# Performance work log

Measured on AMD Instinct MI355X. Metric: run time of the kernel, lower is better.

Reference implementation:

```python
import jax, jax.numpy as jnp
import numpy as np

N, E, IN, HID, H, G, OUT = 50000, 800000, 128, 96, 8, 64, 10
D = HID // H  # per-head dim = 12


def setup_inputs() -> dict:
    key = jax.random.key(0)
    ks = jax.random.split(key, 24)
    s = 0.1
    inp = {
        'x': jax.random.normal(ks[0], (N, IN), jnp.float32),
        'src': jax.random.randint(ks[1], (E,), 0, N, jnp.int32),
        'dst': jax.random.randint(ks[2], (E,), 0, N, jnp.int32),
        'graph_id': jax.random.randint(ks[3], (N,), 0, G, jnp.int32),
        # GraphConv layers (norm='both', weight + bias)
        'W1': jax.random.normal(ks[4], (IN, HID), jnp.float32) * s,
        'b1': jnp.zeros((HID,), jnp.float32),
        'W2': jax.random.normal(ks[5], (HID, HID), jnp.float32) * s,
        'b2': jnp.zeros((HID,), jnp.float32),
        # 3 GATv2 layers, stacked params
        'Ws': jax.random.normal(ks[6], (3, HID, HID), jnp.float32) * s,
        'bs': jnp.zeros((3, HID), jnp.float32),
        'Wd': jax.random.normal(ks[7], (3, HID, HID), jnp.float32) * s,
        'bd': jnp.zeros((3, HID), jnp.float32),
        'attn': jax.random.normal(ks[8], (3, H, D), jnp.float32) * s,
        # classifier MLP (dropout is identity at inference)
        'Wc1': jax.random.normal(ks[9], (HID, HID), jnp.float32) * s,
        'bc1': jnp.zeros((HID,), jnp.float32),
        'Wc2': jax.random.normal(ks[10], (HID, HID // 2), jnp.float32) * s,
        'bc2': jnp.zeros((HID // 2,), jnp.float32),
        'Wc3': jax.random.normal(ks[11], (HID // 2, OUT), jnp.float32) * s,
        'bc3': jnp.zeros((OUT,), jnp.float32),
    }
    return inp


def _graph_conv(h, W, b, src, dst):
    # DGL GraphConv, norm='both', allow_zero_in_degree (degrees clamped to >=1)
    ones = jnp.ones((E,), h.dtype)
    deg_out = jnp.clip(jax.ops.segment_sum(ones, src, N), 1.0)
    deg_in = jnp.clip(jax.ops.segment_sum(ones, dst, N), 1.0)
    h = (h * (deg_out ** -0.5)[:, None]) @ W          # [N, out]
    agg = jax.ops.segment_sum(h[src], dst, N)          # sum over in-edges
    return agg * (deg_in ** -0.5)[:, None] + b


def _gatv2(h, Ws, bs, Wd, bd, attn, src, dst):
    fs = (h @ Ws + bs).reshape(N, H, D)
    fd = (h @ Wd + bd).reshape(N, H, D)
    e = jax.nn.leaky_relu(fs[src] + fd[dst], 0.2)      # [E, H, D]
    logits = jnp.einsum('ehd,hd->eh', e, attn)         # [E, H]
    # edge softmax over incoming edges of each dst node
    m = jax.ops.segment_max(logits, dst, N)            # [N, H]
    ex = jnp.exp(logits - m[dst])
    den = jax.ops.segment_sum(ex, dst, N)              # [N, H]
    a = ex / den[dst]                                  # [E, H]
    rst = jax.ops.segment_sum(a[:, :, None] * fs[src], dst, N)  # [N, H, D]
    return jax.nn.relu(rst).reshape(N, HID)            # activation=relu, then view


def reference(x, src, dst, graph_id, W1, b1, W2, b2, Ws, bs, Wd, bd, attn,
              Wc1, bc1, Wc2, bc2, Wc3, bc3):
    h = jax.nn.relu(_graph_conv(x, W1, b1, src, dst))
    h = jax.nn.relu(_graph_conv(h, W2, b2, src, dst))
    for i in range(3):
        h = _gatv2(h, Ws[i], bs[i], Wd[i], bd[i], attn[i], src, dst)
    # dgl.max_nodes: per-graph max readout
    hg = jax.ops.segment_max(h, graph_id, G)           # [G, HID]
    z = jax.nn.relu(hg @ Wc1 + bc1)
    z = jax.nn.relu(z @ Wc2 + bc2)
    return z @ Wc3 + bc3                               # [G, OUT]
```

## Files before the change

### kernel.cpp

```cpp
#include <hip/hip_runtime.h>
#include <hip/hip_bf16.h>

#define Nn 50000
#define Ee 800000
#define INF_ 128
#define HIDF 96
#define HH 8
#define DD 12
#define GG 64
#define OUTF 10

#define SCAN_CHUNK 512
#define SCAN_BLOCKS ((Nn + SCAN_CHUNK - 1) / SCAN_CHUNK)
#define NSB ((Nn + 255) / 256)
#define RB 128

#define HCHK 256
#define HCHKE (Ee / HCHK)
#define NW 12512
#define DBIN 64

__global__ __launch_bounds__(512) void hist_lds(const int* __restrict__ src,
                                                const int* __restrict__ dst,
                                                unsigned int* __restrict__ partS,
                                                unsigned int* __restrict__ partD,
                                                unsigned char* __restrict__ edge_slot) {
    __shared__ unsigned int hS[NW];
    __shared__ unsigned int hD[NW];
    int b = blockIdx.x, t = threadIdx.x;
    for (int i = t; i < NW; i += 512) { hS[i] = 0u; hD[i] = 0u; }
    __syncthreads();
    int base = b * HCHKE;
    for (int i = t; i < HCHKE; i += 512) {
        int d = dst[base + i];
        unsigned int old = atomicAdd(&hD[d >> 2], 1u << ((d & 3) * 8));
        edge_slot[base + i] = (unsigned char)((old >> ((d & 3) * 8)) & 0xFFu);
        int s = src[base + i];
        atomicAdd(&hS[s >> 2], 1u << ((s & 3) * 8));
    }
    __syncthreads();
    for (int i = t; i < NW; i += 512) {
        partD[(size_t)b * NW + i] = hD[i];
        partS[(size_t)b * NW + i] = hS[i];
    }
}

__global__ __launch_bounds__(256) void hist_scan(unsigned int* __restrict__ partD,
                                                 const unsigned int* __restrict__ partS,
                                                 int* __restrict__ cnt_in,
                                                 float* __restrict__ degI_is,
                                                 float* __restrict__ degO_is,
                                                 int* __restrict__ dcnt) {
    __shared__ int hbin[DBIN];
    int t = threadIdx.x;
    if (t < DBIN) hbin[t] = 0;
    __syncthreads();
    int w = blockIdx.x * 256 + t;
    if (w < NW) {
        unsigned int run = 0u, totS = 0u;
        for (int b = 0; b < HCHK; ++b) {
            size_t idx = (size_t)b * NW + w;
            unsigned int v = partD[idx];
            partD[idx] = run;
            run += v;
            totS += partS[idx];
        }
#pragma unroll
        for (int j = 0; j < 4; ++j) {
            int k = w * 4 + j;
            if (k < Nn) {
                int di = (int)((run >> (j * 8)) & 0xFFu);
                int dо = (int)((totS >> (j * 8)) & 0xFFu);
                cnt_in[k] = di;
                degI_is[k] = rsqrtf((float)max(di, 1));
                degO_is[k] = rsqrtf((float)max(dо, 1));
                atomicAdd(&hbin[DBIN - 1 - min(di, DBIN - 1)], 1);
            }
        }
    }
    __syncthreads();
    if (t < DBIN && hbin[t]) atomicAdd(&dcnt[t], hbin[t]);
}

__global__ __launch_bounds__(256) void scan1_kernel(const int* __restrict__ cnt,
                                                    int* __restrict__ row_start,
                                                    int* __restrict__ blk_sum, int N) {
    __shared__ int part[256];
    int t = threadIdx.x;
    int base = blockIdx.x * SCAN_CHUNK;
    int i0 = base + 2 * t, i1 = i0 + 1;
    int a = (i0 < N) ? cnt[i0] : 0;
    int b = (i1 < N) ? cnt[i1] : 0;
    int s = a + b;
    part[t] = s;
    __syncthreads();
    for (int off = 1; off < 256; off <<= 1) {
        int v = (t >= off) ? part[t - off] : 0;
        __syncthreads();
        part[t] += v;
        __syncthreads();
    }
    int excl = part[t] - s;
    if (i0 < N) row_start[i0] = excl;
    if (i1 < N) row_start[i1] = excl + a;
    if (t == 255) blk_sum[blockIdx.x] = part[255];
}

__global__ __launch_bounds__(128) void scan2_kernel(const int* __restrict__ blk_sum,
                                                    int* __restrict__ blk_off,
                                                    int* __restrict__ row_start,
                                                    const int* __restrict__ dcnt,
                                                    int* __restrict__ dcur, int N) {
    __shared__ int part[128];
    int t = threadIdx.x;
    if (blockIdx.x == 0) {
        int v0 = (t < SCAN_BLOCKS) ? blk_sum[t] : 0;
        part[t] = v0;
        __syncthreads();
        for (int off = 1; off < 128; off <<= 1) {
            int v = (t >= off) ? part[t - off] : 0;
            __syncthreads();
            part[t] += v;
            __syncthreads();
        }
        blk_off[t] = part[t] - v0;
        if (t == 127) row_start[N] = part[127];
    } else {
        int v0 = (t < DBIN) ? dcnt[t] : 0;
        part[t] = v0;
        __syncthreads();
        for (int off = 1; off < DBIN; off <<= 1) {
            int v = (t >= off) ? part[t - off] : 0;
            __syncthreads();
            part[t] += v;
            __syncthreads();
        }
        if (t < DBIN) dcur[t] = part[t] - v0;
    }
}

__global__ __launch_bounds__(256) void scan3_kernel(int* __restrict__ row_start,
                                                    const int* __restrict__ blk_off,
                                                    const int* __restrict__ cnt_in,
                                                    int* __restrict__ dcur,
                                                    int* __restrict__ perm, int N) {
    int t = threadIdx.x;
    if (blockIdx.x < SCAN_BLOCKS) {
        int base = blockIdx.x * SCAN_CHUNK;
        int off = blk_off[blockIdx.x];
        int i0 = base + 2 * t, i1 = i0 + 1;
        if (i0 < N) row_start[i0] += off;
        if (i1 < N) row_start[i1] += off;
    } else {
        __shared__ int lh[DBIN];
        __shared__ int lbase[DBIN];
        if (t < DBIN) lh[t] = 0;
        __syncthreads();
        int n = (blockIdx.x - SCAN_BLOCKS) * 256 + t;
        int bin = 0, lslot = 0;
        if (n < N) {
            bin = DBIN - 1 - min(cnt_in[n], DBIN - 1);
            lslot = atomicAdd(&lh[bin], 1);
        }
        __syncthreads();
        if (t < DBIN) lbase[t] = lh[t] ? atomicAdd(&dcur[t], lh[t]) : 0;
        __syncthreads();
        if (n < N) perm[lbase[bin] + lslot] = n;
    }
}

__global__ __launch_bounds__(512) void fill_kernel(const int* __restrict__ src,
                                                   const int* __restrict__ dst,
                                                   const int* __restrict__ row_start,
                                                   const unsigned int* __restrict__ partD,
                                                   const unsigned char* __restrict__ edge_slot,
                                                   int* __restrict__ csr_src) {
    int b = blockIdx.x, t = threadIdx.x;
    int base = b * HCHKE;
    size_t po = (size_t)b * NW;
    for (int i = t; i < HCHKE; i += 512) {
        int e = base + i;
        int d = dst[e];
        int cb = (int)((partD[po + (d >> 2)] >> ((d & 3) * 8)) & 0xFFu);
        csr_src[row_start[d] + cb + (int)edge_slot[e]] = src[e];
    }
}

__global__ __launch_bounds__(192, 1) void gemm96(const float* __restrict__ A, int K,
                                                 const float* __restrict__ W,
                                                 const float* __restrict__ bias,
                                                 const float* __restrict__ rowScale,
                                                 float* __restrict__ out, int N) {
    __shared__ float W_lds[128 * 96];
    const int t = threadIdx.x;
    const int row0 = blockIdx.x * 64;
    const int tcol = t % 24;
    const int trow = t / 24;

    for (int i = t; i < K * 24; i += 192)
        ((float4*)W_lds)[i] = ((const float4*)W)[i];

    const float* Ap[8];
    float sc[8];
#pragma unroll
    for (int i = 0; i < 8; ++i) {
        int gr = row0 + trow + 8 * i;
        gr = gr < N ? gr : N - 1;
        Ap[i] = A + (size_t)gr * K;
        sc[i] = rowScale ? rowScale[gr] : 1.f;
    }
    float acc[8][4];
#pragma unroll
    for (int i = 0; i < 8; ++i)
#pragma unroll
        for (int j = 0; j < 4; ++j) acc[i][j] = 0.f;

    float4 bufA[8], bufB[8];
#pragma unroll
    for (int i = 0; i < 8; ++i) bufA[i] = *((const float4*)(Ap[i]));

    __syncthreads();

    auto compute = [&](const float4* a, int k) {
#pragma unroll
        for (int kk = 0; kk < 4; ++kk) {
            float4 wv = *((const float4*)(W_lds + (k + kk) * 96 + tcol * 4));
#pragma unroll
            for (int i = 0; i < 8; ++i) {
                float av = ((kk == 0) ? a[i].x : (kk == 1) ? a[i].y
                           : (kk == 2) ? a[i].z : a[i].w) * sc[i];
                acc[i][0] = fmaf(av, wv.x, acc[i][0]);
                acc[i][1] = fmaf(av, wv.y, acc[i][1]);
                acc[i][2] = fmaf(av, wv.z, acc[i][2]);
                acc[i][3] = fmaf(av, wv.w, acc[i][3]);
            }
        }
    };

    for (int k = 0; k + 8 <= K; k += 8) {
#pragma unroll
        for (int i = 0; i < 8; ++i) bufB[i] = *((const float4*)(Ap[i] + k + 4));
        compute(bufA, k);
        if (k + 8 < K) {
#pragma unroll
            for (int i = 0; i < 8; ++i) bufA[i] = *((const float4*)(Ap[i] + k + 8));
        }
        compute(bufB, k + 4);
    }
    float4 b4 = bias ? *((const float4*)(bias + tcol * 4)) : make_float4(0.f, 0.f, 0.f, 0.f);
#pragma unroll
    for (int i = 0; i < 8; ++i) {
        int gr = row0 + trow + 8 * i;
        if (gr < N) {
            float4 o = make_float4(acc[i][0] + b4.x, acc[i][1] + b4.y,
                                   acc[i][2] + b4.z, acc[i][3] + b4.w);
            *((float4*)(out + (size_t)gr * 96 + tcol * 4)) = o;
        }
    }
}

__global__ __launch_bounds__(192, 1) void gemm96x2(const float* __restrict__ A,
                                                   const float* __restrict__ W1_, const float* __restrict__ b1_,
                                                   const float* __restrict__ W2_, const float* __restrict__ b2_,
                                                   float* __restrict__ out1, float* __restrict__ out2, int N) {
    __shared__ float W_lds[2 * 96 * 96];
    const int t = threadIdx.x;
    const int row0 = blockIdx.x * 64;
    const int tcol = t % 24;
    const int trow = t / 24;

    for (int i = t; i < 96 * 24; i += 192) {
        ((float4*)W_lds)[i] = ((const float4*)W1_)[i];
        ((float4*)(W_lds + 96 * 96))[i] = ((const float4*)W2_)[i];
    }

    const float* Ap[8];
#pragma unroll
    for (int i = 0; i < 8; ++i) {
        int gr = row0 + trow + 8 * i;
        gr = gr < N ? gr : N - 1;
        Ap[i] = A + (size_t)gr * 96;
    }
    float acc1[8][4], acc2[8][4];
#pragma unroll
    for (int i = 0; i < 8; ++i)
#pragma unroll
        for (int j = 0; j < 4; ++j) { acc1[i][j] = 0.f; acc2[i][j] = 0.f; }

    float4 bufA[8], bufB[8];
#pragma unroll
    for (int i = 0; i < 8; ++i) bufA[i] = *((const float4*)(Ap[i]));

    __syncthreads();

    auto compute = [&](const float4* a, int k) {
#pragma unroll
        for (int kk = 0; kk < 4; ++kk) {
            float4 wv1 = *((const float4*)(W_lds + (k + kk) * 96 + tcol * 4));
            float4 wv2 = *((const float4*)(W_lds + 96 * 96 + (k + kk) * 96 + tcol * 4));
#pragma unroll
            for (int i = 0; i < 8; ++i) {
                float av = (kk == 0) ? a[i].x : (kk == 1) ? a[i].y : (kk == 2) ? a[i].z : a[i].w;
                acc1[i][0] = fmaf(av, wv1.x, acc1[i][0]);
                acc1[i][1] = fmaf(av, wv1.y, acc1[i][1]);
                acc1[i][2] = fmaf(av, wv1.z, acc1[i][2]);
                acc1[i][3] = fmaf(av, wv1.w, acc1[i][3]);
                acc2[i][0] = fmaf(av, wv2.x, acc2[i][0]);
                acc2[i][1] = fmaf(av, wv2.y, acc2[i][1]);
                acc2[i][2] = fmaf(av, wv2.z, acc2[i][2]);
                acc2[i][3] = fmaf(av, wv2.w, acc2[i][3]);
            }
        }
    };

    for (int k = 0; k + 8 <= 96; k += 8) {
#pragma unroll
        for (int i = 0; i < 8; ++i) bufB[i] = *((const float4*)(Ap[i] + k + 4));
        compute(bufA, k);
        if (k + 8 < 96) {
#pragma unroll
            for (int i = 0; i < 8; ++i) bufA[i] = *((const float4*)(Ap[i] + k + 8));
        }
        compute(bufB, k + 4);
    }
    float4 bb1 = *((const float4*)(b1_ + tcol * 4));
    float4 bb2 = *((const float4*)(b2_ + tcol * 4));
#pragma unroll
    for (int i = 0; i < 8; ++i) {
        int gr = row0 + trow + 8 * i;
        if (gr < N) {
            float4 o1 = make_float4(acc1[i][0] + bb1.x, acc1[i][1] + bb1.y,
                                    acc1[i][2] + bb1.z, acc1[i][3] + bb1.w);
            float4 o2 = make_float4(acc2[i][0] + bb2.x, acc2[i][1] + bb2.y,
                                    acc2[i][2] + bb2.z, acc2[i][3] + bb2.w);
            *((float4*)(out1 + (size_t)gr * 96 + tcol * 4)) = o1;
            *((float4*)(out2 + (size_t)gr * 96 + tcol * 4)) = o2;
        }
    }
}

__global__ __launch_bounds__(192) void gc_agg(const float* __restrict__ hW,
                                              const int* __restrict__ row_start,
                                              const int* __restrict__ csr_src,
                                              const float* __restrict__ degI_is,
                                              const float* __restrict__ bias,
                                              const int* __restrict__ perm,
                                              float* __restrict__ hout, int N) {
    int tid = blockIdx.x * 192 + threadIdx.x;
    int p = tid / 24;
    int c = (tid % 24) * 4;
    if (p >= N) return;
    int n = perm[p];
    int beg = row_start[n], end = row_start[n + 1];
    float4 s = make_float4(0.f, 0.f, 0.f, 0.f);
    int e = beg;
    for (; e + 4 <= end; e += 4) {
        int i0 = csr_src[e], i1 = csr_src[e + 1], i2 = csr_src[e + 2], i3 = csr_src[e + 3];
        float4 v0 = *(const float4*)(hW + (size_t)i0 * 96 + c);
        float4 v1 = *(const float4*)(hW + (size_t)i1 * 96 + c);
        float4 v2 = *(const float4*)(hW + (size_t)i2 * 96 + c);
        float4 v3 = *(const float4*)(hW + (size_t)i3 * 96 + c);
        s.x += (v0.x + v1.x) + (v2.x + v3.x);
        s.y += (v0.y + v1.y) + (v2.y + v3.y);
        s.z += (v0.z + v1.z) + (v2.z + v3.z);
        s.w += (v0.w + v1.w) + (v2.w + v3.w);
    }
    for (; e < end; ++e) {
        int i0 = csr_src[e];
        float4 v0 = *(const float4*)(hW + (size_t)i0 * 96 + c);
        s.x += v0.x; s.y += v0.y; s.z += v0.z; s.w += v0.w;
    }
    float dn = degI_is[n];
    float4 b = *(const float4*)(bias + c);
    float4 o;
    o.x = fmaxf(fmaf(s.x, dn, b.x), 0.f);
    o.y = fmaxf(fmaf(s.y, dn, b.y), 0.f);
    o.z = fmaxf(fmaf(s.z, dn, b.z), 0.f);
    o.w = fmaxf(fmaf(s.w, dn, b.w), 0.f);
    *(float4*)(hout + (size_t)n * 96 + c) = o;
}

__global__ __launch_bounds__(256) void gat_agg(const float* __restrict__ fs,
                                               const float* __restrict__ fd,
                                               const float* __restrict__ attn,
                                               const int* __restrict__ row_start,
                                               const int* __restrict__ csr_src,
                                               const int* __restrict__ perm,
                                               float* __restrict__ hout, int N) {
    int tid = blockIdx.x * 256 + threadIdx.x;
    int p = tid >> 5;
    int hd = (tid >> 2) & 7;
    int q = tid & 3;
    if (p >= N) return;
    int n = perm[p];
    float att[12], fdv[12];
    {
        const float4* ap = (const float4*)(attn + hd * 12);
        float4 a0 = ap[0], a1 = ap[1], a2 = ap[2];
        att[0]=a0.x; att[1]=a0.y; att[2]=a0.z; att[3]=a0.w;
        att[4]=a1.x; att[5]=a1.y; att[6]=a1.z; att[7]=a1.w;
        att[8]=a2.x; att[9]=a2.y; att[10]=a2.z; att[11]=a2.w;
        const float4* dp = (const float4*)(fd + (size_t)n * 96 + hd * 12);
        float4 d0 = dp[0], d1 = dp[1], d2 = dp[2];
        fdv[0]=d0.x; fdv[1]=d0.y; fdv[2]=d0.z; fdv[3]=d0.w;
        fdv[4]=d1.x; fdv[5]=d1.y; fdv[6]=d1.z; fdv[7]=d1.w;
        fdv[8]=d2.x; fdv[9]=d2.y; fdv[10]=d2.z; fdv[11]=d2.w;
    }
    int beg = row_start[n], end = row_start[n + 1];
    float m = -3.0e38f, den = 0.f;
    float A[12];
#pragma unroll
    for (int d = 0; d < 12; ++d) A[d] = 0.f;

    for (int e = beg + q; e < end; e += 4) {
        int i0 = csr_src[e];
        const float4* p0 = (const float4*)(fs + (size_t)i0 * 96 + hd * 12);
        float4 s0 = p0[0], s1 = p0[1], s2 = p0[2];
        float fsv[12];
        fsv[0]=s0.x; fsv[1]=s0.y; fsv[2]=s0.z; fsv[3]=s0.w;
        fsv[4]=s1.x; fsv[5]=s1.y; fsv[6]=s1.z; fsv[7]=s1.w;
        fsv[8]=s2.x; fsv[9]=s2.y; fsv[10]=s2.z; fsv[11]=s2.w;
        float logit = 0.f;
#pragma unroll
        for (int d = 0; d < 12; ++d) {
            float u = fsv[d] + fdv[d];
            u = u > 0.f ? u : 0.2f * u;
            logit = fmaf(u, att[d], logit);
        }
        float nm = fmaxf(m, logit);
        float cc = __expf(m - nm);
        float w  = __expf(logit - nm);
        den = fmaf(den, cc, w);
#pragma unroll
        for (int d = 0; d < 12; ++d) A[d] = fmaf(A[d], cc, w * fsv[d]);
        m = nm;
    }

#pragma unroll
    for (int off = 1; off <= 2; off <<= 1) {
        float m2   = __shfl_xor(m, off, 64);
        float den2 = __shfl_xor(den, off, 64);
        float nm = fmaxf(m, m2);
        float c1 = __expf(m - nm);
        float c2 = __expf(m2 - nm);
        den = den * c1 + den2 * c2;
#pragma unroll
        for (int d = 0; d < 12; ++d) {
            float a2 = __shfl_xor(A[d], off, 64);
            A[d] = A[d] * c1 + a2 * c2;
        }
        m = nm;
    }

    float inv = den > 0.f ? 1.f / den : 0.f;
    float* op = hout + (size_t)n * 96 + hd * 12;
#pragma unroll
    for (int j = 0; j < 3; ++j) {
        int d = q * 3 + j;
        float v = (d == 0) ? A[0] : (d == 1) ? A[1] : (d == 2) ? A[2] : (d == 3) ? A[3]
                : (d == 4) ? A[4] : (d == 5) ? A[5] : (d == 6) ? A[6] : (d == 7) ? A[7]
                : (d == 8) ? A[8] : (d == 9) ? A[9] : (d == 10) ? A[10] : A[11];
        op[d] = fmaxf(v * inv, 0.f);
    }
}

__global__ __launch_bounds__(384) void readout_partial(const float* __restrict__ h,
                                                       const int* __restrict__ graph_id,
                                                       float* __restrict__ partial, int N) {
    __shared__ int lhg[GG * 96];
    int t = threadIdx.x;
    for (int i = t; i < GG * 96; i += 384) lhg[i] = 0;
    __syncthreads();
    int f = t % 96, nl = t / 96;
    for (int n0 = blockIdx.x * 4; n0 < N; n0 += RB * 4) {
        int n = n0 + nl;
        if (n < N) {
            int g = graph_id[n];
            float v = h[(size_t)n * 96 + f];
            atomicMax(&lhg[g * 96 + f], __float_as_int(v));
        }
    }
    __syncthreads();
    for (int i = t; i < GG * 96; i += 384)
        partial[(size_t)blockIdx.x * (GG * 96) + i] = __int_as_float(lhg[i]);
}

__global__ void readout_reduce(const float* __restrict__ partial, float* __restrict__ hg) {
    int i = blockIdx.x * 256 + threadIdx.x;
    if (i < GG * 96) {
        float m = 0.f;
        for (int b = 0; b < RB; ++b) m = fmaxf(m, partial[(size_t)b * (GG * 96) + i]);
        hg[i] = m;
    }
}

__global__ __launch_bounds__(96) void mlp_kernel(const float* __restrict__ hg,
                                                 const float* __restrict__ Wc1, const float* __restrict__ bc1,
                                                 const float* __restrict__ Wc2, const float* __restrict__ bc2,
                                                 const float* __restrict__ Wc3, const float* __restrict__ bc3,
                                                 float* __restrict__ out) {
    int g = blockIdx.x;
    int t = threadIdx.x;
    __shared__ float z0[96], z1[96], z2[48];
    z0[t] = hg[(size_t)g * 96 + t];
    __syncthreads();
    float s = bc1[t];
    for (int k = 0; k < 96; ++k) s = fmaf(z0[k], Wc1[k * 96 + t], s);
    z1[t] = fmaxf(s, 0.f);
    __syncthreads();
    if (t < 48) {
        float s2 = bc2[t];
        for (int k = 0; k < 96; ++k) s2 = fmaf(z1[k], Wc2[k * 48 + t], s2);
        z2[t] = fmaxf(s2, 0.f);
    }
    __syncthreads();
    if (t < 10) {
        float s3 = bc3[t];
        for (int k = 0; k < 48; ++k) s3 = fmaf(z2[k], Wc3[k * 10 + t], s3);
        out[(size_t)g * 10 + t] = s3;
    }
}

extern "C" void kernel_launch(void* const* d_in, const int* in_sizes, int n_in,
                              void* d_out, int out_size, void* d_ws, size_t ws_size,
                              hipStream_t stream) {
    const float* x        = (const float*)d_in[0];
    const int*   src      = (const int*)d_in[1];
    const int*   dst      = (const int*)d_in[2];
    const int*   graph_id = (const int*)d_in[3];
    const float* W1  = (const float*)d_in[4];
    const float* b1  = (const float*)d_in[5];
    const float* W2  = (const float*)d_in[6];
    const float* b2  = (const float*)d_in[7];
    const float* Ws  = (const float*)d_in[8];
    const float* bs  = (const float*)d_in[9];
    const float* Wd  = (const float*)d_in[10];
    const float* bd  = (const float*)d_in[11];
    const float* attn = (const float*)d_in[12];
    const float* Wc1 = (const float*)d_in[13];
    const float* bc1 = (const float*)d_in[14];
    const float* Wc2 = (const float*)d_in[15];
    const float* bc2 = (const float*)d_in[16];
    const float* Wc3 = (const float*)d_in[17];
    const float* bc3 = (const float*)d_in[18];
    float* out = (float*)d_out;

    char* ws = (char*)d_ws;
    size_t off = 0;
    auto alloc = [&](size_t bytes) {
        char* p = ws + off;
        off = (off + bytes + 255) & ~(size_t)255;
        return p;
    };
    int*   cnt_in    = (int*)alloc(Nn * 4);
    int*   row_start = (int*)alloc((Nn + 1) * 4);
    unsigned char* edge_slot = (unsigned char*)alloc(Ee);
    int*   csr_src   = (int*)alloc(Ee * 4);
    int*   perm      = (int*)alloc(Nn * 4);
    float* degI_is   = (float*)alloc(Nn * 4);
    float* degO_is   = (float*)alloc(Nn * 4);
    float* bufH      = (float*)alloc((size_t)Nn * 96 * 4);
    float* bufT      = (float*)alloc((size_t)Nn * 96 * 4);
    float* bufFd     = (float*)alloc((size_t)Nn * 96 * 4);
    float* hg        = (float*)alloc(GG * 96 * 4);
    float* partial   = (float*)alloc((size_t)RB * GG * 96 * 4);
    int*   blk_sum   = (int*)alloc(128 * 4);
    int*   blk_off   = (int*)alloc(128 * 4);
    int*   dcnt      = (int*)alloc(DBIN * 4);
    int*   dcur      = (int*)alloc(DBIN * 4);

    unsigned int* partS = (unsigned int*)bufT;
    unsigned int* partD = (unsigned int*)bufFd;

    hipMemsetAsync(dcnt, 0, DBIN * 4, stream);

    hist_lds<<<HCHK, 512, 0, stream>>>(src, dst, partS, partD, edge_slot);
    hist_scan<<<(NW + 255) / 256, 256, 0, stream>>>(partD, partS, cnt_in, degI_is, degO_is, dcnt);
    scan1_kernel<<<SCAN_BLOCKS, 256, 0, stream>>>(cnt_in, row_start, blk_sum, Nn);
    scan2_kernel<<<2, 128, 0, stream>>>(blk_sum, blk_off, row_start, dcnt, dcur, Nn);
    scan3_kernel<<<SCAN_BLOCKS + NSB, 256, 0, stream>>>(row_start, blk_off, cnt_in, dcur, perm, Nn);
    fill_kernel<<<HCHK, 512, 0, stream>>>(src, dst, row_start, partD, edge_slot, csr_src);

    int gemm_blocks = (Nn + 63) / 64;
    int agg_blocks  = (Nn * 24 + 191) / 192;
    int gat_blocks  = (Nn * 32 + 255) / 256;

    gemm96<<<gemm_blocks, 192, 0, stream>>>(x, 128, W1, nullptr, degO_is, bufT, Nn);
    gc_agg<<<agg_blocks, 192, 0, stream>>>(bufT, row_start, csr_src, degI_is, b1, perm, bufH, Nn);
    gemm96<<<gemm_blocks, 192, 0, stream>>>(bufH, 96, W2, nullptr, degO_is, bufT, Nn);
    gc_agg<<<agg_blocks, 192, 0, stream>>>(bufT, row_start, csr_src, degI_is, b2, perm, bufH, Nn);

    for (int l = 0; l < 3; ++l) {
        const float* Wsl = Ws + (size_t)l * 96 * 96;
        const float* bsl = bs + (size_t)l * 96;
        const float* Wdl = Wd + (size_t)l * 96 * 96;
        const float* bdl = bd + (size_t)l * 96;
        const float* atl = attn + (size_t)l * 96;
        gemm96x2<<<gemm_blocks, 192, 0, stream>>>(bufH, Wsl, bsl, Wdl, bdl, bufT, bufFd, Nn);
        gat_agg<<<gat_blocks, 256, 0, stream>>>(bufT, bufFd, atl, row_start, csr_src, perm, bufH, Nn);
    }

    readout_partial<<<RB, 384, 0, stream>>>(bufH, graph_id, partial, Nn);
    readout_reduce<<<(GG * 96 + 255) / 256, 256, 0, stream>>>(partial, hg);
    mlp_kernel<<<GG, 96, 0, stream>>>(hg, Wc1, bc1, Wc2, bc2, Wc3, bc3, out);
}
```

Before: 640.0 us.

## Rewrite node GEMMs to use wave-uniform scalar weight loads instead of LDS staging

The dense 96-wide GEMMs now map each lane to one row and each wave to a 12-column slice. Because the slice index is wave-uniform (readfirstlane), weight reads can become scalar loads and the LDS staging of W plus the block barrier go away. Blocks grow from 192 to 512 threads and drop the single-block occupancy bound. The cost is that each lane loads its whole A row on its own with strided float4 reads, which coalesce poorly, and every wave re-reads the same A rows.

```diff
diff --git a/kernel.cpp b/kernel.cpp
--- a/kernel.cpp
+++ b/kernel.cpp
@@ -186,155 +186,99 @@
     }
 }
 
-__global__ __launch_bounds__(192, 1) void gemm96(const float* __restrict__ A, int K,
-                                                 const float* __restrict__ W,
-                                                 const float* __restrict__ bias,
-                                                 const float* __restrict__ rowScale,
-                                                 float* __restrict__ out, int N) {
-    __shared__ float W_lds[128 * 96];
+__global__ __launch_bounds__(512) void gemm96(const float* __restrict__ A, int K,
+                                              const float* __restrict__ W,
+                                              const float* __restrict__ bias,
+                                              const float* __restrict__ rowScale,
+                                              float* __restrict__ out, int N) {
     const int t = threadIdx.x;
-    const int row0 = blockIdx.x * 64;
-    const int tcol = t % 24;
-    const int trow = t / 24;
-
-    for (int i = t; i < K * 24; i += 192)
-        ((float4*)W_lds)[i] = ((const float4*)W)[i];
-
-    const float* Ap[8];
-    float sc[8];
-#pragma unroll
-    for (int i = 0; i < 8; ++i) {
-        int gr = row0 + trow + 8 * i;
-        gr = gr < N ? gr : N - 1;
-        Ap[i] = A + (size_t)gr * K;
-        sc[i] = rowScale ? rowScale[gr] : 1.f;
-    }
-    float acc[8][4];
-#pragma unroll
-    for (int i = 0; i < 8; ++i)
-#pragma unroll
-        for (int j = 0; j < 4; ++j) acc[i][j] = 0.f;
-
-    float4 bufA[8], bufB[8];
-#pragma unroll
-    for (int i = 0; i < 8; ++i) bufA[i] = *((const float4*)(Ap[i]));
-
-    __syncthreads();
-
-    auto compute = [&](const float4* a, int k) {
+    const int lane = t & 63;
+    const int cb = __builtin_amdgcn_readfirstlane((t >> 6) * 12);
+    const int row = blockIdx.x * 64 + lane;
+    const int grc = row < N ? row : N - 1;
+    const float* __restrict__ Ap = A + (size_t)grc * K;
+    const float* __restrict__ Wu = W + cb;
+    const float sc = rowScale ? rowScale[grc] : 1.f;
+
+    float acc[12];
+#pragma unroll
+    for (int j = 0; j < 12; ++j) acc[j] = 0.f;
+
+    float4 cur = *((const float4*)Ap);
+    for (int k = 0; k < K; k += 4) {
+        float4 nxt = (k + 4 < K) ? *((const float4*)(Ap + k + 4)) : cur;
 #pragma unroll
         for (int kk = 0; kk < 4; ++kk) {
-            float4 wv = *((const float4*)(W_lds + (k + kk) * 96 + tcol * 4));
-#pragma unroll
-            for (int i = 0; i < 8; ++i) {
-                float av = ((kk == 0) ? a[i].x : (kk == 1) ? a[i].y
-                           : (kk == 2) ? a[i].z : a[i].w) * sc[i];
-                acc[i][0] = fmaf(av, wv.x, acc[i][0]);
-                acc[i][1] = fmaf(av, wv.y, acc[i][1]);
-                acc[i][2] = fmaf(av, wv.z, acc[i][2]);
-                acc[i][3] = fmaf(av, wv.w, acc[i][3]);
+            float av = ((kk == 0) ? cur.x : (kk == 1) ? cur.y : (kk == 2) ? cur.z : cur.w) * sc;
+#pragma unroll
+            for (int j = 0; j < 12; ++j)
+                acc[j] = fmaf(av, Wu[(k + kk) * 96 + j], acc[j]);
+        }
+        cur = nxt;
+    }
+
+    if (row < N) {
+        float* op = out + (size_t)row * 96 + cb;
+#pragma unroll
+        for (int g = 0; g < 3; ++g) {
+            float4 o;
+            o.x = acc[4 * g + 0] + (bias ? bias[cb + 4 * g + 0] : 0.f);
+            o.y = acc[4 * g + 1] + (bias ? bias[cb + 4 * g + 1] : 0.f);
+            o.z = acc[4 * g + 2] + (bias ? bias[cb + 4 * g + 2] : 0.f);
+            o.w = acc[4 * g + 3] + (bias ? bias[cb + 4 * g + 3] : 0.f);
+            *((float4*)(op + 4 * g)) = o;
+        }
+    }
+}
+
+__global__ __launch_bounds__(512) void gemm96x2(const float* __restrict__ A,
+                                                const float* __restrict__ W1_, const float* __restrict__ b1_,
+                                                const float* __restrict__ W2_, const float* __restrict__ b2_,
+                                                float* __restrict__ out1, float* __restrict__ out2, int N) {
+    const int t = threadIdx.x;
+    const int lane = t & 63;
+    const int cb = __builtin_amdgcn_readfirstlane((t >> 6) * 12);
+    const int row = blockIdx.x * 64 + lane;
+    const int grc = row < N ? row : N - 1;
+    const float* __restrict__ Ap = A + (size_t)grc * 96;
+    const float* __restrict__ W1u = W1_ + cb;
+    const float* __restrict__ W2u = W2_ + cb;
+
+    float acc1[12], acc2[12];
+#pragma unroll
+    for (int j = 0; j < 12; ++j) { acc1[j] = 0.f; acc2[j] = 0.f; }
+
+    float4 cur = *((const float4*)Ap);
+    for (int k = 0; k < 96; k += 4) {
+        float4 nxt = (k + 4 < 96) ? *((const float4*)(Ap + k + 4)) : cur;
+#pragma unroll
+        for (int kk = 0; kk < 4; ++kk) {
+            float av = (kk == 0) ? cur.x : (kk == 1) ? cur.y : (kk == 2) ? cur.z : cur.w;
+#pragma unroll
+            for (int j = 0; j < 12; ++j) {
+                acc1[j] = fmaf(av, W1u[(k + kk) * 96 + j], acc1[j]);
+                acc2[j] = fmaf(av, W2u[(k + kk) * 96 + j], acc2[j]);
             }
         }
-    };
-
-    for (int k = 0; k + 8 <= K; k += 8) {
-#pragma unroll
-        for (int i = 0; i < 8; ++i) bufB[i] = *((const float4*)(Ap[i] + k + 4));
-        compute(bufA, k);
-        if (k + 8 < K) {
-#pragma unroll
-            for (int i = 0; i < 8; ++i) bufA[i] = *((const float4*)(Ap[i] + k + 8));
-        }
-        compute(bufB, k + 4);
-    }
-    float4 b4 = bias ? *((const float4*)(bias + tcol * 4)) : make_float4(0.f, 0.f, 0.f, 0.f);
-#pragma unroll
-    for (int i = 0; i < 8; ++i) {
-        int gr = row0 + trow + 8 * i;
-        if (gr < N) {
-            float4 o = make_float4(acc[i][0] + b4.x, acc[i][1] + b4.y,
-                                   acc[i][2] + b4.z, acc[i][3] + b4.w);
-            *((float4*)(out + (size_t)gr * 96 + tcol * 4)) = o;
-        }
-    }
-}
-
-__global__ __launch_bounds__(192, 1) void gemm96x2(const float* __restrict__ A,
-                                                   const float* __restrict__ W1_, const float* __restrict__ b1_,
-                                                   const float* __restrict__ W2_, const float* __restrict__ b2_,
-                                                   float* __restrict__ out1, float* __restrict__ out2, int N) {
-    __shared__ float W_lds[2 * 96 * 96];
-    const int t = threadIdx.x;
-    const int row0 = blockIdx.x * 64;
-    const int tcol = t % 24;
-    const int trow = t / 24;
-
-    for (int i = t; i < 96 * 24; i += 192) {
-        ((float4*)W_lds)[i] = ((const float4*)W1_)[i];
-        ((float4*)(W_lds + 96 * 96))[i] = ((const float4*)W2_)[i];
-    }
-
-    const float* Ap[8];
-#pragma unroll
-    for (int i = 0; i < 8; ++i) {
-        int gr = row0 + trow + 8 * i;
-        gr = gr < N ? gr : N - 1;
-        Ap[i] = A + (size_t)gr * 96;
-    }
-    float acc1[8][4], acc2[8][4];
-#pragma unroll
-    for (int i = 0; i < 8; ++i)
-#pragma unroll
-        for (int j = 0; j < 4; ++j) { acc1[i][j] = 0.f; acc2[i][j] = 0.f; }
-
-    float4 bufA[8], bufB[8];
-#pragma unroll
-    for (int i = 0; i < 8; ++i) bufA[i] = *((const float4*)(Ap[i]));
-
-    __syncthreads();
-
-    auto compute = [&](const float4* a, int k) {
-#pragma unroll
-        for (int kk = 0; kk < 4; ++kk) {
-            float4 wv1 = *((const float4*)(W_lds + (k + kk) * 96 + tcol * 4));
-            float4 wv2 = *((const float4*)(W_lds + 96 * 96 + (k + kk) * 96 + tcol * 4));
-#pragma unroll
-            for (int i = 0; i < 8; ++i) {
-                float av = (kk == 0) ? a[i].x : (kk == 1) ? a[i].y : (kk == 2) ? a[i].z : a[i].w;
-                acc1[i][0] = fmaf(av, wv1.x, acc1[i][0]);
-                acc1[i][1] = fmaf(av, wv1.y, acc1[i][1]);
-                acc1[i][2] = fmaf(av, wv1.z, acc1[i][2]);
-                acc1[i][3] = fmaf(av, wv1.w, acc1[i][3]);
-                acc2[i][0] = fmaf(av, wv2.x, acc2[i][0]);
-                acc2[i][1] = fmaf(av, wv2.y, acc2[i][1]);
-                acc2[i][2] = fmaf(av, wv2.z, acc2[i][2]);
-                acc2[i][3] = fmaf(av, wv2.w, acc2[i][3]);
-            }
-        }
-    };
-
-    for (int k = 0; k + 8 <= 96; k += 8) {
-#pragma unroll
-        for (int i = 0; i < 8; ++i) bufB[i] = *((const float4*)(Ap[i] + k + 4));
-        compute(bufA, k);
-        if (k + 8 < 96) {
-#pragma unroll
-            for (int i = 0; i < 8; ++i) bufA[i] = *((const float4*)(Ap[i] + k + 8));
-        }
-        compute(bufB, k + 4);
-    }
-    float4 bb1 = *((const float4*)(b1_ + tcol * 4));
-    float4 bb2 = *((const float4*)(b2_ + tcol * 4));
-#pragma unroll
-    for (int i = 0; i < 8; ++i) {
-        int gr = row0 + trow + 8 * i;
-        if (gr < N) {
-            float4 o1 = make_float4(acc1[i][0] + bb1.x, acc1[i][1] + bb1.y,
-                                    acc1[i][2] + bb1.z, acc1[i][3] + bb1.w);
-            float4 o2 = make_float4(acc2[i][0] + bb2.x, acc2[i][1] + bb2.y,
-                                    acc2[i][2] + bb2.z, acc2[i][3] + bb2.w);
-            *((float4*)(out1 + (size_t)gr * 96 + tcol * 4)) = o1;
-            *((float4*)(out2 + (size_t)gr * 96 + tcol * 4)) = o2;
+        cur = nxt;
+    }
+
+    if (row < N) {
+        float* op1 = out1 + (size_t)row * 96 + cb;
+        float* op2 = out2 + (size_t)row * 96 + cb;
+#pragma unroll
+        for (int g = 0; g < 3; ++g) {
+            float4 o1, o2;
+            o1.x = acc1[4 * g + 0] + b1_[cb + 4 * g + 0];
+            o1.y = acc1[4 * g + 1] + b1_[cb + 4 * g + 1];
+            o1.z = acc1[4 * g + 2] + b1_[cb + 4 * g + 2];
+            o1.w = acc1[4 * g + 3] + b1_[cb + 4 * g + 3];
+            o2.x = acc2[4 * g + 0] + b2_[cb + 4 * g + 0];
+            o2.y = acc2[4 * g + 1] + b2_[cb + 4 * g + 1];
+            o2.z = acc2[4 * g + 2] + b2_[cb + 4 * g + 2];
+            o2.w = acc2[4 * g + 3] + b2_[cb + 4 * g + 3];
+            *((float4*)(op1 + 4 * g)) = o1;
+            *((float4*)(op2 + 4 * g)) = o2;
         }
     }
 }
@@ -585,9 +529,9 @@
     int agg_blocks  = (Nn * 24 + 191) / 192;
     int gat_blocks  = (Nn * 32 + 255) / 256;
 
-    gemm96<<<gemm_blocks, 192, 0, stream>>>(x, 128, W1, nullptr, degO_is, bufT, Nn);
+    gemm96<<<gemm_blocks, 512, 0, stream>>>(x, 128, W1, nullptr, degO_is, bufT, Nn);
     gc_agg<<<agg_blocks, 192, 0, stream>>>(bufT, row_start, csr_src, degI_is, b1, perm, bufH, Nn);
-    gemm96<<<gemm_blocks, 192, 0, stream>>>(bufH, 96, W2, nullptr, degO_is, bufT, Nn);
+    gemm96<<<gemm_blocks, 512, 0, stream>>>(bufH, 96, W2, nullptr, degO_is, bufT, Nn);
     gc_agg<<<agg_blocks, 192, 0, stream>>>(bufT, row_start, csr_src, degI_is, b2, perm, bufH, Nn);
 
     for (int l = 0; l < 3; ++l) {
@@ -596,7 +540,7 @@
         const float* Wdl = Wd + (size_t)l * 96 * 96;
         const float* bdl = bd + (size_t)l * 96;
         const float* atl = attn + (size_t)l * 96;
-        gemm96x2<<<gemm_blocks, 192, 0, stream>>>(bufH, Wsl, bsl, Wdl, bdl, bufT, bufFd, Nn);
+        gemm96x2<<<gemm_blocks, 512, 0, stream>>>(bufH, Wsl, bsl, Wdl, bdl, bufT, bufFd, Nn);
         gat_agg<<<gat_blocks, 256, 0, stream>>>(bufT, bufFd, atl, row_start, csr_src, perm, bufH, Nn);
     }
 
```

New measurement: 712.7 us. 11.4% more time.

## Chunk weight staging over K in GEMM kernels to cut LDS and raise occupancy

Applied to the files above, without the earlier changes.

The dense GEMM kernels now stage the weight matrix into shared memory in K-chunks (48 rows for gemm96, 24 rows per matrix for the dual GEMM) rather than all at once. The launch-bounds min-blocks hint of 1 is dropped and the register double-buffering of A loads is removed. This shrinks the LDS footprint so more blocks can be resident per CU, which should help hide global-load latency. In exchange it adds a barrier per chunk, reloads weights per chunk, and gives up the explicit prefetch overlap of A loads with FMAs.

```diff
diff --git a/kernel.cpp b/kernel.cpp
--- a/kernel.cpp
+++ b/kernel.cpp
@@ -186,19 +186,17 @@
     }
 }
 
-__global__ __launch_bounds__(192, 1) void gemm96(const float* __restrict__ A, int K,
-                                                 const float* __restrict__ W,
-                                                 const float* __restrict__ bias,
-                                                 const float* __restrict__ rowScale,
-                                                 float* __restrict__ out, int N) {
-    __shared__ float W_lds[128 * 96];
+#define KC 48
+__global__ __launch_bounds__(192) void gemm96(const float* __restrict__ A, int K,
+                                              const float* __restrict__ W,
+                                              const float* __restrict__ bias,
+                                              const float* __restrict__ rowScale,
+                                              float* __restrict__ out, int N) {
+    __shared__ float W_lds[KC * 96];
     const int t = threadIdx.x;
     const int row0 = blockIdx.x * 64;
     const int tcol = t % 24;
     const int trow = t / 24;
-
-    for (int i = t; i < K * 24; i += 192)
-        ((float4*)W_lds)[i] = ((const float4*)W)[i];
 
     const float* Ap[8];
     float sc[8];
@@ -215,37 +213,31 @@
 #pragma unroll
         for (int j = 0; j < 4; ++j) acc[i][j] = 0.f;
 
-    float4 bufA[8], bufB[8];
-#pragma unroll
-    for (int i = 0; i < 8; ++i) bufA[i] = *((const float4*)(Ap[i]));
-
-    __syncthreads();
-
-    auto compute = [&](const float4* a, int k) {
-#pragma unroll
-        for (int kk = 0; kk < 4; ++kk) {
-            float4 wv = *((const float4*)(W_lds + (k + kk) * 96 + tcol * 4));
-#pragma unroll
-            for (int i = 0; i < 8; ++i) {
-                float av = ((kk == 0) ? a[i].x : (kk == 1) ? a[i].y
-                           : (kk == 2) ? a[i].z : a[i].w) * sc[i];
-                acc[i][0] = fmaf(av, wv.x, acc[i][0]);
-                acc[i][1] = fmaf(av, wv.y, acc[i][1]);
-                acc[i][2] = fmaf(av, wv.z, acc[i][2]);
-                acc[i][3] = fmaf(av, wv.w, acc[i][3]);
+    for (int kc = 0; kc < K; kc += KC) {
+        int klen = (K - kc) < KC ? (K - kc) : KC;
+        __syncthreads();
+        for (int i = t; i < klen * 24; i += 192)
+            ((float4*)W_lds)[i] = ((const float4*)W)[kc * 24 + i];
+        __syncthreads();
+        for (int k = 0; k < klen; k += 4) {
+            float4 a[8];
+#pragma unroll
+            for (int i = 0; i < 8; ++i)
+                a[i] = *((const float4*)(Ap[i] + kc + k));
+#pragma unroll
+            for (int kk = 0; kk < 4; ++kk) {
+                float4 wv = *((const float4*)(W_lds + (k + kk) * 96 + tcol * 4));
+#pragma unroll
+                for (int i = 0; i < 8; ++i) {
+                    float av = ((kk == 0) ? a[i].x : (kk == 1) ? a[i].y
+                               : (kk == 2) ? a[i].z : a[i].w) * sc[i];
+                    acc[i][0] = fmaf(av, wv.x, acc[i][0]);
+                    acc[i][1] = fmaf(av, wv.y, acc[i][1]);
+                    acc[i][2] = fmaf(av, wv.z, acc[i][2]);
+                    acc[i][3] = fmaf(av, wv.w, acc[i][3]);
+                }
             }
         }
-    };
-
-    for (int k = 0; k + 8 <= K; k += 8) {
-#pragma unroll
-        for (int i = 0; i < 8; ++i) bufB[i] = *((const float4*)(Ap[i] + k + 4));
-        compute(bufA, k);
-        if (k + 8 < K) {
-#pragma unroll
-            for (int i = 0; i < 8; ++i) bufA[i] = *((const float4*)(Ap[i] + k + 8));
-        }
-        compute(bufB, k + 4);
     }
     float4 b4 = bias ? *((const float4*)(bias + tcol * 4)) : make_float4(0.f, 0.f, 0.f, 0.f);
 #pragma unroll
@@ -259,21 +251,17 @@
     }
 }
 
-__global__ __launch_bounds__(192, 1) void gemm96x2(const float* __restrict__ A,
-                                                   const float* __restrict__ W1_, const float* __restrict__ b1_,
-                                                   const float* __restrict__ W2_, const float* __restrict__ b2_,
-                                                   float* __restrict__ out1, float* __restrict__ out2, int N) {
-    __shared__ float W_lds[2 * 96 * 96];
+#define KC2 24
+__global__ __launch_bounds__(192) void gemm96x2(const float* __restrict__ A,
+                                                const float* __restrict__ W1_, const float* __restrict__ b1_,
+                                                const float* __restrict__ W2_, const float* __restrict__ b2_,
+                                                float* __restrict__ out1, float* __restrict__ out2, int N) {
+    __shared__ float W_lds[2 * KC2 * 96];
     const int t = threadIdx.x;
     const int row0 = blockIdx.x * 64;
     const int tcol = t % 24;
     const int trow = t / 24;
 
-    for (int i = t; i < 96 * 24; i += 192) {
-        ((float4*)W_lds)[i] = ((const float4*)W1_)[i];
-        ((float4*)(W_lds + 96 * 96))[i] = ((const float4*)W2_)[i];
-    }
-
     const float* Ap[8];
 #pragma unroll
     for (int i = 0; i < 8; ++i) {
@@ -287,41 +275,36 @@
 #pragma unroll
         for (int j = 0; j < 4; ++j) { acc1[i][j] = 0.f; acc2[i][j] = 0.f; }
 
-    float4 bufA[8], bufB[8];
-#pragma unroll
-    for (int i = 0; i < 8; ++i) bufA[i] = *((const float4*)(Ap[i]));
-
-    __syncthreads();
-
-    auto compute = [&](const float4* a, int k) {
-#pragma unroll
-        for (int kk = 0; kk < 4; ++kk) {
-            float4 wv1 = *((const float4*)(W_lds + (k + kk) * 96 + tcol * 4));
-            float4 wv2 = *((const float4*)(W_lds + 96 * 96 + (k + kk) * 96 + tcol * 4));
-#pragma unroll
-            for (int i = 0; i < 8; ++i) {
-                float av = (kk == 0) ? a[i].x : (kk == 1) ? a[i].y : (kk == 2) ? a[i].z : a[i].w;
-                acc1[i][0] = fmaf(av, wv1.x, acc1[i][0]);
-                acc1[i][1] = fmaf(av, wv1.y, acc1[i][1]);
-                acc1[i][2] = fmaf(av, wv1.z, acc1[i][2]);
-                acc1[i][3] = fmaf(av, wv1.w, acc1[i][3]);
-                acc2[i][0] = fmaf(av, wv2.x, acc2[i][0]);
-                acc2[i][1] = fmaf(av, wv2.y, acc2[i][1]);
-                acc2[i][2] = fmaf(av, wv2.z, acc2[i][2]);
-                acc2[i][3] = fmaf(av, wv2.w, acc2[i][3]);
+    for (int kc = 0; kc < 96; kc += KC2) {
+        __syncthreads();
+        for (int i = t; i < KC2 * 24; i += 192) {
+            ((float4*)W_lds)[i] = ((const float4*)W1_)[kc * 24 + i];
+            ((float4*)(W_lds + KC2 * 96))[i] = ((const float4*)W2_)[kc * 24 + i];
+        }
+        __syncthreads();
+        for (int k = 0; k < KC2; k += 4) {
+            float4 a[8];
+#pragma unroll
+            for (int i = 0; i < 8; ++i)
+                a[i] = *((const float4*)(Ap[i] + kc + k));
+#pragma unroll
+            for (int kk = 0; kk < 4; ++kk) {
+                float4 wv1 = *((const float4*)(W_lds + (k + kk) * 96 + tcol * 4));
+                float4 wv2 = *((const float4*)(W_lds + KC2 * 96 + (k + kk) * 96 + tcol * 4));
+#pragma unroll
+                for (int i = 0; i < 8; ++i) {
+                    float av = (kk == 0) ? a[i].x : (kk == 1) ? a[i].y : (kk == 2) ? a[i].z : a[i].w;
+                    acc1[i][0] = fmaf(av, wv1.x, acc1[i][0]);
+                    acc1[i][1] = fmaf(av, wv1.y, acc1[i][1]);
+                    acc1[i][2] = fmaf(av, wv1.z, acc1[i][2]);
+                    acc1[i][3] = fmaf(av, wv1.w, acc1[i][3]);
+                    acc2[i][0] = fmaf(av, wv2.x, acc2[i][0]);
+                    acc2[i][1] = fmaf(av, wv2.y, acc2[i][1]);
+                    acc2[i][2] = fmaf(av, wv2.z, acc2[i][2]);
+                    acc2[i][3] = fmaf(av, wv2.w, acc2[i][3]);
+                }
             }
         }
-    };
-
-    for (int k = 0; k + 8 <= 96; k += 8) {
-#pragma unroll
-        for (int i = 0; i < 8; ++i) bufB[i] = *((const float4*)(Ap[i] + k + 4));
-        compute(bufA, k);
-        if (k + 8 < 96) {
-#pragma unroll
-            for (int i = 0; i < 8; ++i) bufA[i] = *((const float4*)(Ap[i] + k + 8));
-        }
-        compute(bufB, k + 4);
     }
     float4 bb1 = *((const float4*)(b1_ + tcol * 4));
     float4 bb2 = *((const float4*)(b2_ + tcol * 4));
```

New measurement: 622.0 us. 2.8% less time.
